# Optimization experiments

Measured on AMD Instinct MI355X. Metric: run time of the kernel, lower is better.

Reference implementation:

```python
import jax, jax.numpy as jnp
import numpy as np

T, B, F = 512, 2048, 16
H1, H2, OUT = 512, 512, 8


def gru_cell(x, h, W_ih, W_hh, b_ih, b_hh):
    # PyTorch nn.GRUCell math. W_ih: [3H, in], W_hh: [3H, H]
    gi = x @ W_ih.T + b_ih
    gh = h @ W_hh.T + b_hh
    i_r, i_z, i_n = jnp.split(gi, 3, axis=-1)
    h_r, h_z, h_n = jnp.split(gh, 3, axis=-1)
    r = jax.nn.sigmoid(i_r + h_r)
    z = jax.nn.sigmoid(i_z + h_z)
    n = jnp.tanh(i_n + r * h_n)
    return (1.0 - z) * n + z * h


def setup_inputs() -> dict:
    key = jax.random.key(0)
    ks = jax.random.split(key, 11)
    s1 = 1.0 / np.sqrt(H1)
    s2 = 1.0 / np.sqrt(H2)
    return {
        "rnn_input": jax.random.normal(ks[0], (T, B, F), dtype=jnp.float32),
        "W_ih0": jax.random.uniform(ks[1], (3 * H1, F), jnp.float32, -s1, s1),
        "W_hh0": jax.random.uniform(ks[2], (3 * H1, H1), jnp.float32, -s1, s1),
        "b_ih0": jax.random.uniform(ks[3], (3 * H1,), jnp.float32, -s1, s1),
        "b_hh0": jax.random.uniform(ks[4], (3 * H1,), jnp.float32, -s1, s1),
        "W_ih1": jax.random.uniform(ks[5], (3 * H2, H1), jnp.float32, -s2, s2),
        "W_hh1": jax.random.uniform(ks[6], (3 * H2, H2), jnp.float32, -s2, s2),
        "b_ih1": jax.random.uniform(ks[7], (3 * H2,), jnp.float32, -s2, s2),
        "b_hh1": jax.random.uniform(ks[8], (3 * H2,), jnp.float32, -s2, s2),
        "W_out": jax.random.uniform(ks[9], (OUT, H2), jnp.float32, -s2, s2),
        "b_out": jax.random.uniform(ks[10], (OUT,), jnp.float32, -s2, s2),
    }


def reference(rnn_input, W_ih0, W_hh0, b_ih0, b_hh0,
              W_ih1, W_hh1, b_ih1, b_hh1, W_out, b_out):
    batch = rnn_input.shape[1]
    h0 = jnp.zeros((batch, H1), dtype=rnn_input.dtype)
    h1 = jnp.zeros((batch, H2), dtype=rnn_input.dtype)

    def step(carry, x_t):
        h0, h1 = carry
        h0 = gru_cell(x_t, h0, W_ih0, W_hh0, b_ih0, b_hh0)
        h1 = gru_cell(h0, h1, W_ih1, W_hh1, b_ih1, b_hh1)
        return (h0, h1), None

    (h0, h1), _ = jax.lax.scan(step, (h0, h1), rnn_input)
    # forward() returns only the output at the final timestep
    return h1 @ W_out.T + b_out
```

## Files before the change

### kernel.cpp

```cpp
#include <hip/hip_runtime.h>

#define DI __device__ __forceinline__

typedef __bf16  bf16x8 __attribute__((ext_vector_type(8)));
typedef float   f32x4  __attribute__((ext_vector_type(4)));
typedef unsigned short u16;
typedef unsigned int   u32;

DI u16 f2bf(float f){ u32 u = __float_as_uint(f); u32 r = 0x7fffu + ((u>>16)&1u); return (u16)((u + r) >> 16); }
DI float bf2f(u16 h){ return __uint_as_float(((u32)h)<<16); }

union U16x8 { u16 u[8]; uint4 v; };
union AB    { uint4 u; bf16x8 b; };

#define MFMA(a,b,c) __builtin_amdgcn_mfma_f32_16x16x32_bf16((a),(b),(c),0,0,0)

DI void gload16(const void* g, void* l){
  __builtin_amdgcn_global_load_lds((const __attribute__((address_space(1))) u32*)g,
                                   (__attribute__((address_space(3))) u32*)l, 16, 0, 0);
}
DI void aload(uint4& d, const void* p){
  asm volatile("global_load_dwordx4 %0, %1, off" : "=&v"(d) : "v"(p) : "memory");
}
template<int N> DI void wait_vmcnt(){ asm volatile("s_waitcnt vmcnt(%0)" :: "n"(N) : "memory"); }
DI void vwait(int n){
  switch(n){
    case 0:  wait_vmcnt<0>();  break;
    case 4:  wait_vmcnt<4>();  break;
    case 8:  wait_vmcnt<8>();  break;
    case 9:  wait_vmcnt<9>();  break;
    case 10: wait_vmcnt<10>(); break;
    default: wait_vmcnt<12>(); break;
  }
}

#define Tn 512
#define Bn 2048
#define Fn 16
#define Hn 512
#define NK32 16

#define OFF_WH0  0ull
#define OFF_WI1  3145728ull
#define OFF_WH1  6291456ull
#define OFF_WI0  9437184ull
#define OFF_H0HI 9633792ull
#define OFF_H0LO 13828096ull
#define OFF_H1HI 18022400ull
#define OFF_H1LO 22216704ull

__global__ __launch_bounds__(256) void prep_w(const float* __restrict__ w0,
                                              const float* __restrict__ w1,
                                              const float* __restrict__ w2,
                                              u16* __restrict__ dst){
  int tid = blockIdx.x*256 + threadIdx.x;
  int p = tid / 98304, rem = tid % 98304;
  int g = rem / 32768, rem2 = rem % 32768;
  int j = rem2 / 64,   k8 = rem2 % 64;
  const float* src = (p==0) ? w0 : ((p==1) ? w1 : w2);
  const float* s = src + (size_t)(g*Hn + j)*Hn + k8*8;
  U16x8 hi, lo;
#pragma unroll
  for (int i=0;i<8;++i){ float v = s[i]; u16 h = f2bf(v); hi.u[i]=h; lo.u[i]=f2bf(v - bf2f(h)); }
  size_t pairidx = (size_t)(g*32 + (j>>4))*16 + (k8>>2);
  u16* d = dst + (size_t)p*1572864 + pairidx*1024 + (size_t)((j&15) + (k8&3)*16)*8;
  *(uint4*)d = hi.v;
  *(uint4*)(d + 512) = lo.v;
}

__global__ __launch_bounds__(256) void prep_wi0(const float* __restrict__ w,
                                                u16* __restrict__ dst){
  int tid = blockIdx.x*256 + threadIdx.x;
  int g = tid / 2048, j = (tid % 2048) >> 2, k8 = tid & 3;
  U16x8 hi, lo;
  if (k8 < 2){
    const float* s = w + (size_t)(g*Hn + j)*Fn + k8*8;
#pragma unroll
    for (int i=0;i<8;++i){ float v = s[i]; u16 h = f2bf(v); hi.u[i]=h; lo.u[i]=f2bf(v - bf2f(h)); }
  } else {
#pragma unroll
    for (int i=0;i<8;++i){ hi.u[i]=0; lo.u[i]=0; }
  }
  size_t pairidx = (size_t)(g*32 + (j>>4));
  u16* d = dst + pairidx*1024 + (size_t)((j&15) + k8*16)*8;
  *(uint4*)d = hi.v;
  *(uint4*)(d + 512) = lo.v;
}

__global__ __launch_bounds__(256) void zero_ws(char* __restrict__ ws){
  int tid = blockIdx.x*256 + threadIdx.x;
  uint4 z = {0u,0u,0u,0u};
  int region = tid >> 17;
  int off = tid & 131071;
  size_t base = (region==0) ? OFF_H0HI : (region==1) ? OFF_H0LO
              : (region==2) ? OFF_H1HI : OFF_H1LO;
  *(uint4*)(ws + base + (size_t)off*16) = z;
}

template<int IS_L0>
__global__ __launch_bounds__(256, 2) void gru_step(
    const u16* __restrict__ Wi, const u16* __restrict__ Wh,
    const float* __restrict__ xsrc,
    const u16* __restrict__ Ai_hi, const u16* __restrict__ Ai_lo,
    const u16* __restrict__ Ah_hi, const u16* __restrict__ Ah_lo,
    const float* __restrict__ b_ih, const float* __restrict__ b_hh,
    u16* __restrict__ hout_hi, u16* __restrict__ hout_lo)
{
  constexpr int NI = IS_L0 ? 1 : 16;
  constexpr int NT = IS_L0 ? 17 : 32;
  __shared__ __align__(16) char smem[45056];
  const int tid  = threadIdx.x;
  const int lane = tid & 63, wv = tid >> 6;
  const int bid = blockIdx.x;
  const int mt = (bid & 7)*2 + ((bid >> 3) & 1);
  const int jt = bid >> 4;

  f32x4 acc[2][4];
#pragma unroll
  for (int m=0;m<2;++m)
#pragma unroll
    for (int o=0;o<4;++o){ f32x4 z = {0.f,0.f,0.f,0.f}; acc[m][o] = z; }

  if (IS_L0){
    int b_loc = tid >> 1, kh = tid & 1;
    const float* xs = xsrc + (size_t)(mt*128 + b_loc)*Fn + kh*8;
    U16x8 u;
#pragma unroll
    for (int i=0;i<8;++i) u.u[i] = f2bf(xs[i]);
    char* dst = smem + 36864 + (b_loc>>4)*1024 + (size_t)((b_loc&15) + kh*16)*16;
    *(uint4*)dst = u.v;
    uint4 z = {0u,0u,0u,0u};
    *(uint4*)(dst + 512) = z;
  }

  uint4 areg[16];

  auto issueW = [&](int s){
    char* buf = smem + (s % 6)*6144;
    bool ish = (s >= NI);
    const u16* w; int nk, k32w;
    if (IS_L0 && !ish){ w = Wi; nk = 1; k32w = 0; }
    else { w = ish ? Wh : Wi; nk = NK32; k32w = ish ? (s - NI) : s; }
    int ntask = (wv < 2) ? 2 : 1;
    int tbase = (wv < 2) ? wv*2 : (2 + wv);
    for (int ii=0; ii<ntask; ++ii){
      int task = tbase + ii, g = task >> 1, hl = task & 1;
      size_t go = ((size_t)((g*32 + jt)*nk + k32w))*1024 + (size_t)hl*512 + (size_t)lane*8;
      gload16(w + go, buf + task*1024);
    }
  };

  auto issueA = [&](int s, uint4* dst){
    bool ish = (s >= NI);
    if (IS_L0 && !ish) return;
    int k32 = ish ? (s - NI) : s;
    const u16* ahi = ish ? Ah_hi : Ai_hi;
    const u16* alo = ish ? Ah_lo : Ai_lo;
#pragma unroll
    for (int m=0;m<2;++m){
      size_t go = ((size_t)((mt*8 + wv*2 + m)*NK32 + k32))*512 + (size_t)lane*8;
      aload(dst[m*2],   ahi + go);
      aload(dst[m*2+1], alo + go);
    }
  };

  auto compute = [&](int t, const uint4* ar){
    const char* buf = smem + (t % 6)*6144;
    bf16x8 w[3][2];
#pragma unroll
    for (int g=0; g<3; ++g)
#pragma unroll
      for (int hl=0; hl<2; ++hl)
        w[g][hl] = *(const bf16x8*)(buf + (g*2+hl)*1024 + lane*16);
    bool ish = (t >= NI);
    if (IS_L0 && t==0){
#pragma unroll
      for (int m=0;m<2;++m){
        bf16x8 ax = *(const bf16x8*)(smem + 36864 + (wv*2+m)*1024 + lane*16);
        acc[m][0] = MFMA(ax, w[0][0], acc[m][0]); acc[m][0] = MFMA(ax, w[0][1], acc[m][0]);
        acc[m][1] = MFMA(ax, w[1][0], acc[m][1]); acc[m][1] = MFMA(ax, w[1][1], acc[m][1]);
        acc[m][2] = MFMA(ax, w[2][0], acc[m][2]); acc[m][2] = MFMA(ax, w[2][1], acc[m][2]);
      }
    } else {
#pragma unroll
      for (int m=0;m<2;++m){
        AB cah, cal; cah.u = ar[m*2]; cal.u = ar[m*2+1];
        bf16x8 ah = cah.b, al = cal.b;
        acc[m][0] = MFMA(ah, w[0][0], acc[m][0]);
        acc[m][0] = MFMA(ah, w[0][1], acc[m][0]);
        acc[m][0] = MFMA(al, w[0][0], acc[m][0]);
        acc[m][1] = MFMA(ah, w[1][0], acc[m][1]);
        acc[m][1] = MFMA(ah, w[1][1], acc[m][1]);
        acc[m][1] = MFMA(al, w[1][0], acc[m][1]);
        if (!ish){
          acc[m][2] = MFMA(ah, w[2][0], acc[m][2]);
          acc[m][2] = MFMA(ah, w[2][1], acc[m][2]);
          acc[m][2] = MFMA(al, w[2][0], acc[m][2]);
        } else {
          acc[m][3] = MFMA(ah, w[2][0], acc[m][3]);
          acc[m][3] = MFMA(ah, w[2][1], acc[m][3]);
          acc[m][3] = MFMA(al, w[2][0], acc[m][3]);
        }
      }
    }
  };

  issueW(0); issueW(1); issueW(2); issueW(3); issueW(4);
  issueA(0, &areg[0]); issueA(1, &areg[4]); issueA(2, &areg[8]);
  asm volatile("s_waitcnt lgkmcnt(0)" ::: "memory");

#pragma unroll
  for (int t=0; t<NT; ++t){
    int d = NT-1-t;
    int lv01, lv23;
    if      (t==0){ lv01=8;  lv23=8; }
    else if (t==1){ lv01=10; lv23=9; }
    else if (d>=4){ lv01=12; lv23=10; }
    else if (d==3){ lv01=10; lv23=9; }
    else if (d==2){ lv01=8;  lv23=8; }
    else if (d==1){ lv01=4;  lv23=4; }
    else          { lv01=0;  lv23=0; }
    if (wv < 2) vwait(lv01); else vwait(lv23);
    __builtin_amdgcn_sched_barrier(0);
    __builtin_amdgcn_s_barrier();
    compute(t, &areg[(t&3)*4]);
    if (t+5 < NT) issueW(t+5);
    if (t+3 < NT) issueA(t+3, &areg[((t+3)&3)*4]);
  }

  const int col = lane & 15, rg = lane >> 4;
  const int j = jt*16 + col;
  const float bir = b_ih[j], biz = b_ih[Hn + j], bin = b_ih[2*Hn + j];
  const float bhr = b_hh[j], bhz = b_hh[Hn + j], bhn = b_hh[2*Hn + j];
#pragma unroll
  for (int m=0;m<2;++m){
    int brow = mt*128 + wv*32 + m*16 + rg*4;
#pragma unroll
    for (int r=0;r<4;++r){
      int b = brow + r;
      float pr  = acc[m][0][r] + bir + bhr;
      float pz  = acc[m][1][r] + biz + bhz;
      float pin = acc[m][2][r] + bin;
      float phn = acc[m][3][r] + bhn;
      float rgt = 1.f/(1.f + __expf(-pr));
      float zgt = 1.f/(1.f + __expf(-pz));
      float e2  = __expf(2.f*(pin + rgt*phn));
      float nn  = 1.f - 2.f/(e2 + 1.f);
      size_t fo = ((size_t)(b>>4)*NK32 + (j>>5))*512 + (size_t)((b&15) + ((j>>3)&3)*16)*8 + (j&7);
      float hv  = bf2f(Ah_hi[fo]) + bf2f(Ah_lo[fo]);
      float hnv = (1.f - zgt)*nn + zgt*hv;
      u16 hi = f2bf(hnv);
      u16 lo = f2bf(hnv - bf2f(hi));
      hout_hi[fo] = hi; hout_lo[fo] = lo;
    }
  }
}

__global__ __launch_bounds__(64) void outproj(const u16* __restrict__ h1hi,
                                              const u16* __restrict__ h1lo,
                                              const float* __restrict__ Wout,
                                              const float* __restrict__ bout,
                                              float* __restrict__ out){
  int b = blockIdx.x, l = threadIdx.x;
  float a[8] = {0.f,0.f,0.f,0.f,0.f,0.f,0.f,0.f};
  for (int jj = l; jj < Hn; jj += 64){
    size_t fo = ((size_t)(b>>4)*NK32 + (jj>>5))*512 + (size_t)((b&15) + ((jj>>3)&3)*16)*8 + (jj&7);
    float hv = bf2f(h1hi[fo]) + bf2f(h1lo[fo]);
#pragma unroll
    for (int o=0;o<8;++o) a[o] += hv * Wout[o*Hn + jj];
  }
#pragma unroll
  for (int o=0;o<8;++o){
#pragma unroll
    for (int off=32; off; off>>=1) a[o] += __shfl_xor(a[o], off);
  }
  if (l == 0){
#pragma unroll
    for (int o=0;o<8;++o) out[b*8+o] = a[o] + bout[o];
  }
}

extern "C" void kernel_launch(void* const* d_in, const int* in_sizes, int n_in,
                              void* d_out, int out_size, void* d_ws, size_t ws_size,
                              hipStream_t stream){
  (void)in_sizes; (void)n_in; (void)out_size; (void)ws_size;
  const float* x    = (const float*)d_in[0];
  const float* Wih0 = (const float*)d_in[1];
  const float* Whh0 = (const float*)d_in[2];
  const float* bih0 = (const float*)d_in[3];
  const float* bhh0 = (const float*)d_in[4];
  const float* Wih1 = (const float*)d_in[5];
  const float* Whh1 = (const float*)d_in[6];
  const float* bih1 = (const float*)d_in[7];
  const float* bhh1 = (const float*)d_in[8];
  const float* Wout = (const float*)d_in[9];
  const float* bout = (const float*)d_in[10];
  char* ws = (char*)d_ws;

  u16* WH0 = (u16*)(ws + OFF_WH0);
  const u16* WI1 = (const u16*)(ws + OFF_WI1);
  const u16* WH1 = (const u16*)(ws + OFF_WH1);
  const u16* WI0 = (const u16*)(ws + OFF_WI0);
  u16 *H0HI = (u16*)(ws + OFF_H0HI), *H0LO = (u16*)(ws + OFF_H0LO);
  u16 *H1HI = (u16*)(ws + OFF_H1HI), *H1LO = (u16*)(ws + OFF_H1LO);

  prep_w  <<<1152, 256, 0, stream>>>(Whh0, Wih1, Whh1, WH0);
  prep_wi0<<<  24, 256, 0, stream>>>(Wih0, (u16*)(ws + OFF_WI0));
  zero_ws <<<2048, 256, 0, stream>>>(ws);

  for (int s = 0; s < Tn; ++s){
    int rp = s & 1, wp = rp ^ 1;
    gru_step<1><<<512, 256, 0, stream>>>(
        WI0, (const u16*)WH0,
        x + (size_t)s*Bn*Fn,
        nullptr, nullptr,
        H0HI + (size_t)rp*1048576, H0LO + (size_t)rp*1048576,
        bih0, bhh0,
        H0HI + (size_t)wp*1048576, H0LO + (size_t)wp*1048576);
    gru_step<0><<<512, 256, 0, stream>>>(
        WI1, WH1,
        nullptr,
        H0HI + (size_t)wp*1048576, H0LO + (size_t)wp*1048576,
        H1HI + (size_t)rp*1048576, H1LO + (size_t)rp*1048576,
        bih1, bhh1,
        H1HI + (size_t)wp*1048576, H1LO + (size_t)wp*1048576);
  }

  outproj<<<2048, 64, 0, stream>>>(
      H1HI, H1LO, Wout, bout, (float*)d_out);
}
```

Measured before the change: 17.92 ms.

## Replace per-step kernel launches with a persistent kernel using flag-based sync

Replaces the 1024 per-timestep kernel launches with one persistent kernel of 256 blocks that loops over all timesteps. Blocks synchronise per batch tile through atomic counters in global memory, and hidden-state stores and loads bypass caches (sc0 sc1) so they are visible across blocks. Each block now computes 32 output columns instead of 16 and keeps the previous hidden state in registers instead of reloading it. This removes launch overhead and device-wide barriers, at the cost of spin-wait latency, one block per CU, and a deadlock risk if the 256 blocks are not all co-resident.

Result: slower. 24.93 ms (+39.1%).

```diff
diff --git a/kernel.cpp b/kernel.cpp
--- a/kernel.cpp
+++ b/kernel.cpp
@@ -20,18 +20,24 @@
                                    (__attribute__((address_space(3))) u32*)l, 16, 0, 0);
 }
 DI void aload(uint4& d, const void* p){
-  asm volatile("global_load_dwordx4 %0, %1, off" : "=&v"(d) : "v"(p) : "memory");
+  asm volatile("global_load_dwordx4 %0, %1, off sc0 sc1" : "=&v"(d) : "v"(p) : "memory");
+}
+DI void sstore16(void* p, u16 v){
+  asm volatile("global_store_short %0, %1, off sc0 sc1" :: "v"(p), "v"((u32)v) : "memory");
 }
 template<int N> DI void wait_vmcnt(){ asm volatile("s_waitcnt vmcnt(%0)" :: "n"(N) : "memory"); }
 DI void vwait(int n){
   switch(n){
     case 0:  wait_vmcnt<0>();  break;
-    case 4:  wait_vmcnt<4>();  break;
+    case 7:  wait_vmcnt<7>();  break;
     case 8:  wait_vmcnt<8>();  break;
-    case 9:  wait_vmcnt<9>();  break;
-    case 10: wait_vmcnt<10>(); break;
-    default: wait_vmcnt<12>(); break;
-  }
+    case 11: wait_vmcnt<11>(); break;
+    default: wait_vmcnt<14>(); break;
+  }
+}
+DI void spinf(u32* f){
+  while (__hip_atomic_load(f, __ATOMIC_RELAXED, __HIP_MEMORY_SCOPE_AGENT) < 16u)
+    __builtin_amdgcn_s_sleep(8);
 }
 
 #define Tn 512
@@ -40,14 +46,15 @@
 #define Hn 512
 #define NK32 16
 
-#define OFF_WH0  0ull
-#define OFF_WI1  3145728ull
-#define OFF_WH1  6291456ull
-#define OFF_WI0  9437184ull
-#define OFF_H0HI 9633792ull
-#define OFF_H0LO 13828096ull
-#define OFF_H1HI 18022400ull
-#define OFF_H1LO 22216704ull
+#define OFF_WH0   0ull
+#define OFF_WI1   3145728ull
+#define OFF_WH1   6291456ull
+#define OFF_WI0   9437184ull
+#define OFF_H0HI  9633792ull
+#define OFF_H0LO  13828096ull
+#define OFF_H1HI  18022400ull
+#define OFF_H1LO  22216704ull
+#define OFF_FLAGS 26411008ull
 
 __global__ __launch_bounds__(256) void prep_w(const float* __restrict__ w0,
                                               const float* __restrict__ w1,
@@ -90,72 +97,73 @@
 __global__ __launch_bounds__(256) void zero_ws(char* __restrict__ ws){
   int tid = blockIdx.x*256 + threadIdx.x;
   uint4 z = {0u,0u,0u,0u};
-  int region = tid >> 17;
-  int off = tid & 131071;
-  size_t base = (region==0) ? OFF_H0HI : (region==1) ? OFF_H0LO
-              : (region==2) ? OFF_H1HI : OFF_H1LO;
-  *(uint4*)(ws + base + (size_t)off*16) = z;
-}
-
-template<int IS_L0>
-__global__ __launch_bounds__(256, 2) void gru_step(
-    const u16* __restrict__ Wi, const u16* __restrict__ Wh,
-    const float* __restrict__ xsrc,
-    const u16* __restrict__ Ai_hi, const u16* __restrict__ Ai_lo,
-    const u16* __restrict__ Ah_hi, const u16* __restrict__ Ah_lo,
-    const float* __restrict__ b_ih, const float* __restrict__ b_hh,
-    u16* __restrict__ hout_hi, u16* __restrict__ hout_lo)
+  size_t o;
+  if      (tid < 131072) o = OFF_H0HI + 2097152 + (size_t)tid*16;
+  else if (tid < 262144) o = OFF_H0LO + 2097152 + (size_t)(tid-131072)*16;
+  else if (tid < 393216) o = OFF_H1HI + 2097152 + (size_t)(tid-262144)*16;
+  else if (tid < 524288) o = OFF_H1LO + 2097152 + (size_t)(tid-393216)*16;
+  else                   o = OFF_FLAGS + (size_t)(tid-524288)*16;
+  *(uint4*)(ws + o) = z;
+}
+
+struct Ctx {
+  const u16 *Wi, *Wh;
+  const u16 *Ahi_i, *Alo_i, *Ahi_h, *Alo_h;
+  u16 *Ohi, *Olo;
+  const float* xs;
+};
+
+struct PArgs {
+  const u16 *Wi0, *Wh0, *Wi1, *Wh1;
+  const float *x, *bi0, *bh0, *bi1, *bh1;
+  u16 *H0HI, *H0LO, *H1HI, *H1LO;
+  u32 *flags;
+};
+
+template<int LAY>
+DI void layer_step(const Ctx& c, char* smem, int tid, int lane, int wv,
+                   int mt, int jt,
+                   f32x4 (&hprev)[2][2],
+                   const float (&SR)[2], const float (&SZ)[2],
+                   const float (&BIN)[2], const float (&BHN)[2],
+                   u32* sp1, u32* sp2, u32* pub)
 {
-  constexpr int NI = IS_L0 ? 1 : 16;
-  constexpr int NT = IS_L0 ? 17 : 32;
-  __shared__ __align__(16) char smem[45056];
-  const int tid  = threadIdx.x;
-  const int lane = tid & 63, wv = tid >> 6;
-  const int bid = blockIdx.x;
-  const int mt = (bid & 7)*2 + ((bid >> 3) & 1);
-  const int jt = bid >> 4;
-
-  f32x4 acc[2][4];
+  constexpr int NI = (LAY==0) ? 1 : 16;
+  constexpr int NT = (LAY==0) ? 17 : 32;
+
+  f32x4 acc[2][2][4];
 #pragma unroll
   for (int m=0;m<2;++m)
 #pragma unroll
-    for (int o=0;o<4;++o){ f32x4 z = {0.f,0.f,0.f,0.f}; acc[m][o] = z; }
-
-  if (IS_L0){
-    int b_loc = tid >> 1, kh = tid & 1;
-    const float* xs = xsrc + (size_t)(mt*128 + b_loc)*Fn + kh*8;
-    U16x8 u;
-#pragma unroll
-    for (int i=0;i<8;++i) u.u[i] = f2bf(xs[i]);
-    char* dst = smem + 36864 + (b_loc>>4)*1024 + (size_t)((b_loc&15) + kh*16)*16;
-    *(uint4*)dst = u.v;
-    uint4 z = {0u,0u,0u,0u};
-    *(uint4*)(dst + 512) = z;
-  }
+    for (int cg=0;cg<2;++cg)
+#pragma unroll
+      for (int o=0;o<4;++o){ f32x4 z={0.f,0.f,0.f,0.f}; acc[m][cg][o]=z; }
 
   uint4 areg[16];
 
-  auto issueW = [&](int s){
-    char* buf = smem + (s % 6)*6144;
-    bool ish = (s >= NI);
-    const u16* w; int nk, k32w;
-    if (IS_L0 && !ish){ w = Wi; nk = 1; k32w = 0; }
-    else { w = ish ? Wh : Wi; nk = NK32; k32w = ish ? (s - NI) : s; }
-    int ntask = (wv < 2) ? 2 : 1;
-    int tbase = (wv < 2) ? wv*2 : (2 + wv);
-    for (int ii=0; ii<ntask; ++ii){
-      int task = tbase + ii, g = task >> 1, hl = task & 1;
-      size_t go = ((size_t)((g*32 + jt)*nk + k32w))*1024 + (size_t)hl*512 + (size_t)lane*8;
+  auto issueW = [&](int tt){
+    char* buf = smem + (tt & 3)*12288;
+    bool ish = tt >= NI;
+    const u16* w; int nk, k32;
+    if (LAY==0 && !ish){ w = c.Wi; nk = 1; k32 = 0; }
+    else if (!ish)     { w = c.Wi; nk = NK32; k32 = tt; }
+    else               { w = c.Wh; nk = NK32; k32 = tt - NI; }
+#pragma unroll
+    for (int ii=0; ii<3; ++ii){
+      int task = wv*3 + ii;
+      int g = task>>2, cg = (task>>1)&1, hl = task&1;
+      size_t go = ((size_t)((g*32 + jt*2 + cg)*nk + k32))*1024 + (size_t)hl*512 + (size_t)lane*8;
       gload16(w + go, buf + task*1024);
     }
   };
 
-  auto issueA = [&](int s, uint4* dst){
-    bool ish = (s >= NI);
-    if (IS_L0 && !ish) return;
-    int k32 = ish ? (s - NI) : s;
-    const u16* ahi = ish ? Ah_hi : Ai_hi;
-    const u16* alo = ish ? Ah_lo : Ai_lo;
+  auto issueA = [&](int tt){
+    uint4* dst = &areg[(tt & 3)*4];
+    bool ish = tt >= NI;
+    const u16 *ahi, *alo; int k32;
+    if (LAY==0 && !ish){ ahi = c.Ahi_h; alo = c.Alo_h; k32 = 0; }
+    else if (!ish)     { ahi = c.Ahi_i; alo = c.Alo_i; k32 = tt; }
+    else               { ahi = c.Ahi_h; alo = c.Alo_h; k32 = tt - NI; }
 #pragma unroll
     for (int m=0;m<2;++m){
       size_t go = ((size_t)((mt*8 + wv*2 + m)*NK32 + k32))*512 + (size_t)lane*8;
@@ -164,94 +172,166 @@
     }
   };
 
-  auto compute = [&](int t, const uint4* ar){
-    const char* buf = smem + (t % 6)*6144;
-    bf16x8 w[3][2];
-#pragma unroll
-    for (int g=0; g<3; ++g)
-#pragma unroll
-      for (int hl=0; hl<2; ++hl)
-        w[g][hl] = *(const bf16x8*)(buf + (g*2+hl)*1024 + lane*16);
-    bool ish = (t >= NI);
-    if (IS_L0 && t==0){
-#pragma unroll
-      for (int m=0;m<2;++m){
-        bf16x8 ax = *(const bf16x8*)(smem + 36864 + (wv*2+m)*1024 + lane*16);
-        acc[m][0] = MFMA(ax, w[0][0], acc[m][0]); acc[m][0] = MFMA(ax, w[0][1], acc[m][0]);
-        acc[m][1] = MFMA(ax, w[1][0], acc[m][1]); acc[m][1] = MFMA(ax, w[1][1], acc[m][1]);
-        acc[m][2] = MFMA(ax, w[2][0], acc[m][2]); acc[m][2] = MFMA(ax, w[2][1], acc[m][2]);
-      }
-    } else {
-#pragma unroll
-      for (int m=0;m<2;++m){
-        AB cah, cal; cah.u = ar[m*2]; cal.u = ar[m*2+1];
-        bf16x8 ah = cah.b, al = cal.b;
-        acc[m][0] = MFMA(ah, w[0][0], acc[m][0]);
-        acc[m][0] = MFMA(ah, w[0][1], acc[m][0]);
-        acc[m][0] = MFMA(al, w[0][0], acc[m][0]);
-        acc[m][1] = MFMA(ah, w[1][0], acc[m][1]);
-        acc[m][1] = MFMA(ah, w[1][1], acc[m][1]);
-        acc[m][1] = MFMA(al, w[1][0], acc[m][1]);
-        if (!ish){
-          acc[m][2] = MFMA(ah, w[2][0], acc[m][2]);
-          acc[m][2] = MFMA(ah, w[2][1], acc[m][2]);
-          acc[m][2] = MFMA(al, w[2][0], acc[m][2]);
-        } else {
-          acc[m][3] = MFMA(ah, w[2][0], acc[m][3]);
-          acc[m][3] = MFMA(ah, w[2][1], acc[m][3]);
-          acc[m][3] = MFMA(al, w[2][0], acc[m][3]);
-        }
-      }
-    }
-  };
-
-  issueW(0); issueW(1); issueW(2); issueW(3); issueW(4);
-  issueA(0, &areg[0]); issueA(1, &areg[4]); issueA(2, &areg[8]);
+  if (LAY==0){
+    int row = tid >> 1, half = tid & 1;
+    const float* xsrc = c.xs + (size_t)(mt*128 + row)*Fn + half*8;
+    U16x8 u;
+#pragma unroll
+    for (int i=0;i<8;++i) u.u[i] = f2bf(xsrc[i]);
+    char* dst = smem + 49152 + (row>>4)*1024 + (size_t)((row&15) + half*16)*16;
+    *(uint4*)dst = u.v;
+    uint4 z = {0u,0u,0u,0u};
+    char* dz = smem + 49152 + (row>>4)*1024 + (size_t)((row&15) + (half+2)*16)*16;
+    *(uint4*)dz = z;
+  }
+
+  issueW(0); issueW(1); issueW(2);
+  if (tid == 0){
+    if (sp1) spinf(sp1);
+    if (sp2) spinf(sp2);
+  }
   asm volatile("s_waitcnt lgkmcnt(0)" ::: "memory");
+  __builtin_amdgcn_sched_barrier(0);
+  __builtin_amdgcn_s_barrier();
+  __builtin_amdgcn_sched_barrier(0);
+  issueA(0); issueA(1); issueA(2);
 
 #pragma unroll
   for (int t=0; t<NT; ++t){
-    int d = NT-1-t;
-    int lv01, lv23;
-    if      (t==0){ lv01=8;  lv23=8; }
-    else if (t==1){ lv01=10; lv23=9; }
-    else if (d>=4){ lv01=12; lv23=10; }
-    else if (d==3){ lv01=10; lv23=9; }
-    else if (d==2){ lv01=8;  lv23=8; }
-    else if (d==1){ lv01=4;  lv23=4; }
-    else          { lv01=0;  lv23=0; }
-    if (wv < 2) vwait(lv01); else vwait(lv23);
+    int lvl = (t==0) ? 8 : (t==1) ? 11 : (t==NT-1) ? 0 : (t==NT-2) ? 7 : 14;
+    vwait(lvl);
     __builtin_amdgcn_sched_barrier(0);
     __builtin_amdgcn_s_barrier();
-    compute(t, &areg[(t&3)*4]);
-    if (t+5 < NT) issueW(t+5);
-    if (t+3 < NT) issueA(t+3, &areg[((t+3)&3)*4]);
+    __builtin_amdgcn_sched_barrier(0);
+    {
+      const char* buf = smem + (t & 3)*12288;
+      bool ish = t >= NI;
+      bf16x8 a_hi[2], a_lo[2];
+      if (!(LAY==0 && t==0)){
+        const uint4* ar = &areg[(t & 3)*4];
+        AB u0,u1,u2,u3;
+        u0.u=ar[0]; u1.u=ar[1]; u2.u=ar[2]; u3.u=ar[3];
+        a_hi[0]=u0.b; a_lo[0]=u1.b; a_hi[1]=u2.b; a_lo[1]=u3.b;
+      } else {
+        a_hi[0] = *(const bf16x8*)(smem + 49152 + (wv*2+0)*1024 + lane*16);
+        a_hi[1] = *(const bf16x8*)(smem + 49152 + (wv*2+1)*1024 + lane*16);
+      }
+#pragma unroll
+      for (int g=0; g<3; ++g)
+#pragma unroll
+        for (int cg=0; cg<2; ++cg){
+          bf16x8 whi = *(const bf16x8*)(buf + (g*4+cg*2+0)*1024 + lane*16);
+          bf16x8 wlo = *(const bf16x8*)(buf + (g*4+cg*2+1)*1024 + lane*16);
+          int gi = (g<2) ? g : (ish ? 3 : 2);
+#pragma unroll
+          for (int m=0;m<2;++m){
+            if (LAY==0 && t==0){
+              acc[m][cg][gi] = MFMA(a_hi[m], whi, acc[m][cg][gi]);
+              acc[m][cg][gi] = MFMA(a_hi[m], wlo, acc[m][cg][gi]);
+            } else {
+              acc[m][cg][gi] = MFMA(a_hi[m], whi, acc[m][cg][gi]);
+              acc[m][cg][gi] = MFMA(a_hi[m], wlo, acc[m][cg][gi]);
+              acc[m][cg][gi] = MFMA(a_lo[m], whi, acc[m][cg][gi]);
+            }
+          }
+        }
+    }
+    if (t+3 < NT){ issueW(t+3); issueA(t+3); }
   }
 
   const int col = lane & 15, rg = lane >> 4;
-  const int j = jt*16 + col;
-  const float bir = b_ih[j], biz = b_ih[Hn + j], bin = b_ih[2*Hn + j];
-  const float bhr = b_hh[j], bhz = b_hh[Hn + j], bhn = b_hh[2*Hn + j];
-#pragma unroll
-  for (int m=0;m<2;++m){
-    int brow = mt*128 + wv*32 + m*16 + rg*4;
-#pragma unroll
-    for (int r=0;r<4;++r){
-      int b = brow + r;
-      float pr  = acc[m][0][r] + bir + bhr;
-      float pz  = acc[m][1][r] + biz + bhz;
-      float pin = acc[m][2][r] + bin;
-      float phn = acc[m][3][r] + bhn;
-      float rgt = 1.f/(1.f + __expf(-pr));
-      float zgt = 1.f/(1.f + __expf(-pz));
-      float e2  = __expf(2.f*(pin + rgt*phn));
-      float nn  = 1.f - 2.f/(e2 + 1.f);
-      size_t fo = ((size_t)(b>>4)*NK32 + (j>>5))*512 + (size_t)((b&15) + ((j>>3)&3)*16)*8 + (j&7);
-      float hv  = bf2f(Ah_hi[fo]) + bf2f(Ah_lo[fo]);
-      float hnv = (1.f - zgt)*nn + zgt*hv;
-      u16 hi = f2bf(hnv);
-      u16 lo = f2bf(hnv - bf2f(hi));
-      hout_hi[fo] = hi; hout_lo[fo] = lo;
+#pragma unroll
+  for (int m=0;m<2;++m)
+#pragma unroll
+    for (int cg=0;cg<2;++cg){
+      int j = jt*32 + cg*16 + col;
+      size_t foj = (size_t)(j>>5)*512 + (size_t)((j>>3)&3)*128 + (size_t)(j&7);
+#pragma unroll
+      for (int r=0;r<4;++r){
+        int b = mt*128 + wv*32 + m*16 + rg*4 + r;
+        float pr  = acc[m][cg][0][r] + SR[cg];
+        float pz  = acc[m][cg][1][r] + SZ[cg];
+        float pin = acc[m][cg][2][r] + BIN[cg];
+        float phn = acc[m][cg][3][r] + BHN[cg];
+        float rgt = 1.f/(1.f + __expf(-pr));
+        float zgt = 1.f/(1.f + __expf(-pz));
+        float e2  = __expf(2.f*(pin + rgt*phn));
+        float nn  = 1.f - 2.f/(e2 + 1.f);
+        float hv  = hprev[m][cg][r];
+        float hnv = (1.f - zgt)*nn + zgt*hv;
+        hprev[m][cg][r] = hnv;
+        u16 hi = f2bf(hnv);
+        u16 lo = f2bf(hnv - bf2f(hi));
+        size_t fo = (size_t)(b>>4)*NK32*512 + foj + (size_t)(b&15)*8;
+        sstore16(c.Ohi + fo, hi);
+        sstore16(c.Olo + fo, lo);
+      }
+    }
+  asm volatile("s_waitcnt vmcnt(0)" ::: "memory");
+  __builtin_amdgcn_sched_barrier(0);
+  __builtin_amdgcn_s_barrier();
+  if (tid == 0) atomicAdd(pub, 1u);
+}
+
+__global__ __launch_bounds__(256, 1) void gru_persist(PArgs a){
+  __shared__ __align__(16) char smem[86016];
+  const int tid = threadIdx.x, lane = tid & 63, wv = tid >> 6;
+  const int bid = blockIdx.x;
+  const int mt = (bid & 7)*2 + ((bid >> 3) & 1);
+  const int jt = bid >> 4;
+  const int col = lane & 15;
+
+  float SR[2][2], SZ[2][2], BIN[2][2], BHN[2][2];
+#pragma unroll
+  for (int cg=0; cg<2; ++cg){
+    int j = jt*32 + cg*16 + col;
+    SR[0][cg]  = a.bi0[j] + a.bh0[j];
+    SZ[0][cg]  = a.bi0[Hn+j] + a.bh0[Hn+j];
+    BIN[0][cg] = a.bi0[2*Hn+j];
+    BHN[0][cg] = a.bh0[2*Hn+j];
+    SR[1][cg]  = a.bi1[j] + a.bh1[j];
+    SZ[1][cg]  = a.bi1[Hn+j] + a.bh1[Hn+j];
+    BIN[1][cg] = a.bi1[2*Hn+j];
+    BHN[1][cg] = a.bh1[2*Hn+j];
+  }
+  f32x4 hp0[2][2], hp1[2][2];
+#pragma unroll
+  for (int m=0;m<2;++m)
+#pragma unroll
+    for (int cg=0;cg<2;++cg){ f32x4 z={0.f,0.f,0.f,0.f}; hp0[m][cg]=z; hp1[m][cg]=z; }
+
+#pragma unroll 1
+  for (int s=0; s<Tn; ++s){
+    int p = s & 1;
+    {
+      Ctx c;
+      c.Wi = a.Wi0; c.Wh = a.Wh0;
+      c.Ahi_i = a.H0HI; c.Alo_i = a.H0LO;
+      c.Ahi_h = a.H0HI + (size_t)(p^1)*1048576;
+      c.Alo_h = a.H0LO + (size_t)(p^1)*1048576;
+      c.Ohi   = a.H0HI + (size_t)p*1048576;
+      c.Olo   = a.H0LO + (size_t)p*1048576;
+      c.xs    = a.x + (size_t)s*Bn*Fn;
+      u32* w1 = (s>0) ? &a.flags[(size_t)(s-1)*16 + mt] : nullptr;
+      layer_step<0>(c, smem, tid, lane, wv, mt, jt, hp0,
+                    SR[0], SZ[0], BIN[0], BHN[0],
+                    w1, nullptr, &a.flags[(size_t)s*16 + mt]);
+    }
+    {
+      Ctx c;
+      c.Wi = a.Wi1; c.Wh = a.Wh1;
+      c.Ahi_i = a.H0HI + (size_t)p*1048576;
+      c.Alo_i = a.H0LO + (size_t)p*1048576;
+      c.Ahi_h = a.H1HI + (size_t)(p^1)*1048576;
+      c.Alo_h = a.H1LO + (size_t)(p^1)*1048576;
+      c.Ohi   = a.H1HI + (size_t)p*1048576;
+      c.Olo   = a.H1LO + (size_t)p*1048576;
+      c.xs    = nullptr;
+      u32* w1 = &a.flags[(size_t)s*16 + mt];
+      u32* w2 = (s>0) ? &a.flags[(size_t)(512 + s - 1)*16 + mt] : nullptr;
+      layer_step<1>(c, smem, tid, lane, wv, mt, jt, hp1,
+                    SR[1], SZ[1], BIN[1], BHN[1],
+                    w1, w2, &a.flags[(size_t)(512 + s)*16 + mt]);
     }
   }
 }
@@ -297,35 +377,24 @@
   const float* bout = (const float*)d_in[10];
   char* ws = (char*)d_ws;
 
-  u16* WH0 = (u16*)(ws + OFF_WH0);
-  const u16* WI1 = (const u16*)(ws + OFF_WI1);
-  const u16* WH1 = (const u16*)(ws + OFF_WH1);
-  const u16* WI0 = (const u16*)(ws + OFF_WI0);
-  u16 *H0HI = (u16*)(ws + OFF_H0HI), *H0LO = (u16*)(ws + OFF_H0LO);
-  u16 *H1HI = (u16*)(ws + OFF_H1HI), *H1LO = (u16*)(ws + OFF_H1LO);
-
-  prep_w  <<<1152, 256, 0, stream>>>(Whh0, Wih1, Whh1, WH0);
+  prep_w  <<<1152, 256, 0, stream>>>(Whh0, Wih1, Whh1, (u16*)(ws + OFF_WH0));
   prep_wi0<<<  24, 256, 0, stream>>>(Wih0, (u16*)(ws + OFF_WI0));
-  zero_ws <<<2048, 256, 0, stream>>>(ws);
-
-  for (int s = 0; s < Tn; ++s){
-    int rp = s & 1, wp = rp ^ 1;
-    gru_step<1><<<512, 256, 0, stream>>>(
-        WI0, (const u16*)WH0,
-        x + (size_t)s*Bn*Fn,
-        nullptr, nullptr,
-        H0HI + (size_t)rp*1048576, H0LO + (size_t)rp*1048576,
-        bih0, bhh0,
-        H0HI + (size_t)wp*1048576, H0LO + (size_t)wp*1048576);
-    gru_step<0><<<512, 256, 0, stream>>>(
-        WI1, WH1,
-        nullptr,
-        H0HI + (size_t)wp*1048576, H0LO + (size_t)wp*1048576,
-        H1HI + (size_t)rp*1048576, H1LO + (size_t)rp*1048576,
-        bih1, bhh1,
-        H1HI + (size_t)wp*1048576, H1LO + (size_t)wp*1048576);
-  }
+  zero_ws <<<2064, 256, 0, stream>>>(ws);
+
+  PArgs pa;
+  pa.Wi0 = (const u16*)(ws + OFF_WI0);
+  pa.Wh0 = (const u16*)(ws + OFF_WH0);
+  pa.Wi1 = (const u16*)(ws + OFF_WI1);
+  pa.Wh1 = (const u16*)(ws + OFF_WH1);
+  pa.x = x; pa.bi0 = bih0; pa.bh0 = bhh0; pa.bi1 = bih1; pa.bh1 = bhh1;
+  pa.H0HI = (u16*)(ws + OFF_H0HI); pa.H0LO = (u16*)(ws + OFF_H0LO);
+  pa.H1HI = (u16*)(ws + OFF_H1HI); pa.H1LO = (u16*)(ws + OFF_H1LO);
+  pa.flags = (u32*)(ws + OFF_FLAGS);
+
+  gru_persist<<<256, 256, 0, stream>>>(pa);
 
   outproj<<<2048, 64, 0, stream>>>(
-      H1HI, H1LO, Wout, bout, (float*)d_out);
-}
+      (const u16*)(ws + OFF_H1HI) + 1048576,
+      (const u16*)(ws + OFF_H1LO) + 1048576,
+      Wout, bout, (float*)d_out);
+}
```
